# Kernel tuning notes

Measured on AMD Instinct MI355X. Metric: run time of the kernel, lower is better.

Reference implementation:

```python
import jax, jax.numpy as jnp
import numpy as np

LN_EPS = 1e-5


def setup_inputs() -> dict:
    key = jax.random.key(0)
    ks = jax.random.split(key, 4)
    B, S, H, R = 8, 4096, 1024, 64
    hidden_states = jax.random.normal(ks[0], (B, S, H), dtype=jnp.float32)
    w_down = jax.random.normal(ks[1], (H, R), dtype=jnp.float32) * (1.0 / np.sqrt(H))
    b_down = jnp.zeros((R,), dtype=jnp.float32)
    w_up = jax.random.normal(ks[2], (R, H), dtype=jnp.float32) * (1.0 / np.sqrt(R))
    b_up = jnp.zeros((H,), dtype=jnp.float32)
    ln_gamma = jnp.ones((H,), dtype=jnp.float32)
    ln_beta = jnp.zeros((H,), dtype=jnp.float32)
    return {
        "hidden_states": hidden_states,
        "ln_gamma": ln_gamma,
        "ln_beta": ln_beta,
        "w_down": w_down,
        "b_down": b_down,
        "w_up": w_up,
        "b_up": b_up,
    }


def _layernorm(x, gamma, beta):
    mu = jnp.mean(x, axis=-1, keepdims=True)
    var = jnp.mean(jnp.square(x - mu), axis=-1, keepdims=True)
    return (x - mu) * jax.lax.rsqrt(var + LN_EPS) * gamma + beta


def reference(hidden_states, ln_gamma, ln_beta, w_down, b_down, w_up, b_up):
    # pre-norm adapter: LN -> down-proj -> gelu -> up-proj -> +residual
    res = hidden_states
    h = _layernorm(hidden_states, ln_gamma, ln_beta)
    h = jnp.einsum("bsh,hr->bsr", h, w_down) + b_down
    h = jax.nn.gelu(h, approximate=False)  # torch GELU (exact erf form)
    h = jnp.einsum("bsr,rh->bsh", h, w_up) + b_up
    return h + res
```

## Files before the change

### kernel.cpp

```cpp
#include <hip/hip_runtime.h>
#include <hip/hip_bf16.h>
#include <math.h>

#define H 1024
#define R 64
#define NTHREADS 256
#define TSTRIDE 72

typedef __attribute__((ext_vector_type(8))) short short8;
typedef __attribute__((ext_vector_type(4))) float floatx4;

__device__ __forceinline__ unsigned short f2bf(float f) {
    unsigned int u = __builtin_bit_cast(unsigned int, f);
    u += 0x7fffu + ((u >> 16) & 1u);
    return (unsigned short)(u >> 16);
}

__global__ void prep(const float* __restrict__ w_down,
                     const float* __restrict__ w_up,
                     const float* __restrict__ gamma,
                     const float* __restrict__ beta,
                     const float* __restrict__ b_down,
                     unsigned short* __restrict__ wsd,
                     unsigned short* __restrict__ wsu,
                     float* __restrict__ w1, float* __restrict__ c0) {
    __shared__ float red[8];
    int bid = blockIdx.x;
    if (bid < 256) {
        int tid = bid * NTHREADS + threadIdx.x;
        int j    = tid & 7;
        int lane = (tid >> 3) & 63;
        int f    = tid >> 9;
        int b = lane >> 4, p = lane & 15;
        {
            int kk = f >> 2, n = f & 3;
            int row = kk * 32 + b * 8 + j;
            int col = n * 16 + p;
            wsd[tid] = f2bf(gamma[row] * w_down[row * R + col]);
        }
        {
            int ks = f >> 6, n = f & 63;
            int row = ks * 32 + b * 8 + j;
            int col = n * 16 + p;
            wsu[tid] = f2bf(w_up[row * H + col]);
        }
    } else {
        int r = bid - 256;
        int t = threadIdx.x;
        float a = 0.f, c = 0.f;
        for (int h = t; h < H; h += NTHREADS) {
            float wd = w_down[h * R + r];
            a += gamma[h] * wd;
            c += beta[h] * wd;
        }
        #pragma unroll
        for (int off = 32; off >= 1; off >>= 1) {
            a += __shfl_xor(a, off);
            c += __shfl_xor(c, off);
        }
        int wv = t >> 6;
        if ((t & 63) == 0) { red[wv] = a; red[4 + wv] = c; }
        __syncthreads();
        if (t == 0) {
            w1[r] = red[0] + red[1] + red[2] + red[3];
            c0[r] = red[4] + red[5] + red[6] + red[7] + b_down[r];
        }
    }
}

__global__ __launch_bounds__(NTHREADS, 2)
void adapter_kernel(const float* __restrict__ x,
                    const float* __restrict__ b_up,
                    const unsigned short* __restrict__ wsd,
                    const unsigned short* __restrict__ wsu,
                    const float* __restrict__ w1v,
                    const float* __restrict__ c0v,
                    float* __restrict__ out) {
    __shared__ __align__(16) unsigned short t_lds[4][16 * TSTRIDE];

    const int tid  = threadIdx.x;
    const int lane = tid & 63;
    const int w    = tid >> 6;
    const int p    = lane & 15;
    const int b    = lane >> 4;
    const long row0 = (long)blockIdx.x * 64 + w * 16;

    float s1 = 0.f, s2 = 0.f;
    floatx4 acc[4];
    #pragma unroll
    for (int nt = 0; nt < 4; ++nt) acc[nt] = floatx4{0.f, 0.f, 0.f, 0.f};

    const float* xw = x + (row0 + p) * H + b * 8;
    const short8* wsd8 = (const short8*)wsd;

    floatx4 bx0[8], bx1[8];
    short8 wd[2][4];
    #pragma unroll
    for (int i = 0; i < 8; ++i) {
        bx0[i] = *(const floatx4*)(xw + i * 32);
        bx1[i] = *(const floatx4*)(xw + i * 32 + 4);
    }
    #pragma unroll
    for (int nt = 0; nt < 4; ++nt) {
        wd[0][nt] = wsd8[(size_t)nt * 64 + lane];
        wd[1][nt] = wsd8[(size_t)(4 + nt) * 64 + lane];
    }

    for (int ko = 0; ko < 3; ++ko) {
        #pragma unroll
        for (int ki = 0; ki < 8; ++ki) {
            const int kt = ko * 8 + ki;
            floatx4 v0 = bx0[ki], v1 = bx1[ki];
            bx0[ki] = *(const floatx4*)(xw + (kt + 8) * 32);
            bx1[ki] = *(const floatx4*)(xw + (kt + 8) * 32 + 4);
            short8 wl[4];
            #pragma unroll
            for (int nt = 0; nt < 4; ++nt) {
                wl[nt] = wd[ki & 1][nt];
                wd[ki & 1][nt] = wsd8[(size_t)((kt + 2) * 4 + nt) * 64 + lane];
            }
            short8 a;
            #pragma unroll
            for (int e = 0; e < 4; ++e) {
                s1 += v0[e] + v1[e];
                s2 += v0[e] * v0[e] + v1[e] * v1[e];
                a[e]     = (short)f2bf(v0[e]);
                a[4 + e] = (short)f2bf(v1[e]);
            }
            #pragma unroll
            for (int nt = 0; nt < 4; ++nt)
                acc[nt] = __builtin_amdgcn_mfma_f32_16x16x32_bf16(a, wl[nt], acc[nt], 0, 0, 0);
        }
    }
    #pragma unroll
    for (int ki = 0; ki < 8; ++ki) {
        const int kt = 24 + ki;
        floatx4 v0 = bx0[ki], v1 = bx1[ki];
        short8 wl[4];
        #pragma unroll
        for (int nt = 0; nt < 4; ++nt) {
            wl[nt] = wd[ki & 1][nt];
            if (ki < 6)
                wd[ki & 1][nt] = wsd8[(size_t)((kt + 2) * 4 + nt) * 64 + lane];
        }
        short8 a;
        #pragma unroll
        for (int e = 0; e < 4; ++e) {
            s1 += v0[e] + v1[e];
            s2 += v0[e] * v0[e] + v1[e] * v1[e];
            a[e]     = (short)f2bf(v0[e]);
            a[4 + e] = (short)f2bf(v1[e]);
        }
        #pragma unroll
        for (int nt = 0; nt < 4; ++nt)
            acc[nt] = __builtin_amdgcn_mfma_f32_16x16x32_bf16(a, wl[nt], acc[nt], 0, 0, 0);
    }

    s1 += __shfl_xor(s1, 16); s1 += __shfl_xor(s1, 32);
    s2 += __shfl_xor(s2, 16); s2 += __shfl_xor(s2, 32);
    float mu = s1 * (1.0f / (float)H);
    float var = s2 * (1.0f / (float)H) - mu * mu;
    float rs = rsqrtf(var + 1e-5f);

    #pragma unroll
    for (int reg = 0; reg < 4; ++reg) {
        float mur = __shfl(mu, b * 4 + reg);
        float rsr = __shfl(rs, b * 4 + reg);
        #pragma unroll
        for (int nt = 0; nt < 4; ++nt) {
            int col = nt * 16 + p;
            float u = rsr * (acc[nt][reg] - mur * w1v[col]) + c0v[col];
            u = 0.5f * u * (1.0f + erff(u * 0.70710678f));
            t_lds[w][(b * 4 + reg) * TSTRIDE + col] = f2bf(u);
        }
    }

    const short8* wsu8 = (const short8*)wsu;
    const long rbase = row0 + b * 4;
    short8 wq0[8], wq1[8];
    float bb[8], rx0[8], rx1[8], rx2[8], rx3[8];
    #pragma unroll
    for (int i = 0; i < 8; ++i) {
        wq0[i] = wsu8[(size_t)i * 64 + lane];
        wq1[i] = wsu8[(size_t)(64 + i) * 64 + lane];
        int col = i * 16 + p;
        bb[i]  = b_up[col];
        rx0[i] = x[(rbase + 0) * H + col];
        rx1[i] = x[(rbase + 1) * H + col];
        rx2[i] = x[(rbase + 2) * H + col];
        rx3[i] = x[(rbase + 3) * H + col];
    }
    __syncthreads();
    short8 a0 = *(const short8*)&t_lds[w][p * TSTRIDE + b * 8];
    short8 a1 = *(const short8*)&t_lds[w][p * TSTRIDE + 32 + b * 8];

    for (int no = 0; no < 7; ++no) {
        #pragma unroll
        for (int ni = 0; ni < 8; ++ni) {
            const int n = no * 8 + ni;
            short8 bu0 = wq0[ni], bu1 = wq1[ni];
            float bup = bb[ni];
            float r0 = rx0[ni], r1 = rx1[ni], r2 = rx2[ni], r3 = rx3[ni];
            const int nc = n + 8;
            const int colc = nc * 16 + p;
            wq0[ni] = wsu8[(size_t)nc * 64 + lane];
            wq1[ni] = wsu8[(size_t)(64 + nc) * 64 + lane];
            bb[ni]  = b_up[colc];
            rx0[ni] = x[(rbase + 0) * H + colc];
            rx1[ni] = x[(rbase + 1) * H + colc];
            rx2[ni] = x[(rbase + 2) * H + colc];
            rx3[ni] = x[(rbase + 3) * H + colc];
            floatx4 av = {0.f, 0.f, 0.f, 0.f};
            av = __builtin_amdgcn_mfma_f32_16x16x32_bf16(a0, bu0, av, 0, 0, 0);
            av = __builtin_amdgcn_mfma_f32_16x16x32_bf16(a1, bu1, av, 0, 0, 0);
            const int col = n * 16 + p;
            out[(rbase + 0) * H + col] = av[0] + bup + r0;
            out[(rbase + 1) * H + col] = av[1] + bup + r1;
            out[(rbase + 2) * H + col] = av[2] + bup + r2;
            out[(rbase + 3) * H + col] = av[3] + bup + r3;
        }
    }
    #pragma unroll
    for (int ni = 0; ni < 8; ++ni) {
        const int n = 56 + ni;
        short8 bu0 = wq0[ni], bu1 = wq1[ni];
        floatx4 av = {0.f, 0.f, 0.f, 0.f};
        av = __builtin_amdgcn_mfma_f32_16x16x32_bf16(a0, bu0, av, 0, 0, 0);
        av = __builtin_amdgcn_mfma_f32_16x16x32_bf16(a1, bu1, av, 0, 0, 0);
        const int col = n * 16 + p;
        out[(rbase + 0) * H + col] = av[0] + bb[ni] + rx0[ni];
        out[(rbase + 1) * H + col] = av[1] + bb[ni] + rx1[ni];
        out[(rbase + 2) * H + col] = av[2] + bb[ni] + rx2[ni];
        out[(rbase + 3) * H + col] = av[3] + bb[ni] + rx3[ni];
    }
}

extern "C" void kernel_launch(void* const* d_in, const int* in_sizes, int n_in,
                              void* d_out, int out_size, void* d_ws, size_t ws_size,
                              hipStream_t stream) {
    const float* x      = (const float*)d_in[0];
    const float* gamma  = (const float*)d_in[1];
    const float* beta   = (const float*)d_in[2];
    const float* w_down = (const float*)d_in[3];
    const float* b_down = (const float*)d_in[4];
    const float* w_up   = (const float*)d_in[5];
    const float* b_up   = (const float*)d_in[6];
    float* out = (float*)d_out;

    unsigned short* wsd = (unsigned short*)d_ws;
    unsigned short* wsu = wsd + 65536;
    float* w1 = (float*)(wsu + 65536);
    float* c0 = w1 + 64;

    int M = in_sizes[0] / H;
    prep<<<320, NTHREADS, 0, stream>>>(w_down, w_up, gamma, beta, b_down,
                                       wsd, wsu, w1, c0);
    adapter_kernel<<<M / 64, NTHREADS, 0, stream>>>(x, b_up, wsd, wsu, w1, c0, out);
}
```

Before: 278.2 us.

## Stage adapter weights through double-buffered LDS via global_load_lds

Down- and up-projection weight fragments are now loaded cooperatively into double-buffered LDS with the direct global-to-LDS load builtin. Each wave previously fetched every weight fragment itself into registers. This cuts redundant global/L2 weight traffic across the four waves and frees registers that held prefetched weights. In exchange it adds a __syncthreads per chunk, uses 32KB more LDS (which may lower occupancy), and shortens the x prefetch depth in the down-projection loop.

```diff
diff --git a/kernel.cpp b/kernel.cpp
--- a/kernel.cpp
+++ b/kernel.cpp
@@ -9,6 +9,10 @@
 
 typedef __attribute__((ext_vector_type(8))) short short8;
 typedef __attribute__((ext_vector_type(4))) float floatx4;
+
+#define GLD_LDS(gp, lp) \
+    __builtin_amdgcn_global_load_lds((const __attribute__((address_space(1))) void*)(gp), \
+                                     (__attribute__((address_space(3))) void*)(lp), 16, 0, 0)
 
 __device__ __forceinline__ unsigned short f2bf(float f) {
     unsigned int u = __builtin_bit_cast(unsigned int, f);
@@ -76,6 +80,7 @@
                     const float* __restrict__ w1v,
                     const float* __restrict__ c0v,
                     float* __restrict__ out) {
+    __shared__ __align__(16) unsigned short wbuf[2][8192];
     __shared__ __align__(16) unsigned short t_lds[4][16 * TSTRIDE];
 
     const int tid  = threadIdx.x;
@@ -84,76 +89,62 @@
     const int p    = lane & 15;
     const int b    = lane >> 4;
     const long row0 = (long)blockIdx.x * 64 + w * 16;
+    const float* xw = x + (row0 + p) * H + b * 8;
 
     float s1 = 0.f, s2 = 0.f;
     floatx4 acc[4];
     #pragma unroll
     for (int nt = 0; nt < 4; ++nt) acc[nt] = floatx4{0.f, 0.f, 0.f, 0.f};
 
-    const float* xw = x + (row0 + p) * H + b * 8;
-    const short8* wsd8 = (const short8*)wsd;
-
-    floatx4 bx0[8], bx1[8];
-    short8 wd[2][4];
-    #pragma unroll
-    for (int i = 0; i < 8; ++i) {
-        bx0[i] = *(const floatx4*)(xw + i * 32);
-        bx1[i] = *(const floatx4*)(xw + i * 32 + 4);
-    }
-    #pragma unroll
-    for (int nt = 0; nt < 4; ++nt) {
-        wd[0][nt] = wsd8[(size_t)nt * 64 + lane];
-        wd[1][nt] = wsd8[(size_t)(4 + nt) * 64 + lane];
-    }
-
-    for (int ko = 0; ko < 3; ++ko) {
-        #pragma unroll
-        for (int ki = 0; ki < 8; ++ki) {
-            const int kt = ko * 8 + ki;
-            floatx4 v0 = bx0[ki], v1 = bx1[ki];
-            bx0[ki] = *(const floatx4*)(xw + (kt + 8) * 32);
-            bx1[ki] = *(const floatx4*)(xw + (kt + 8) * 32 + 4);
-            short8 wl[4];
-            #pragma unroll
-            for (int nt = 0; nt < 4; ++nt) {
-                wl[nt] = wd[ki & 1][nt];
-                wd[ki & 1][nt] = wsd8[(size_t)((kt + 2) * 4 + nt) * 64 + lane];
-            }
+    auto stage_d = [&](int c, int buf) {
+        #pragma unroll
+        for (int i = 0; i < 4; ++i) {
+            int fl = w * 4 + i;
+            GLD_LDS(wsd + ((size_t)(c * 16 + fl) * 64 + lane) * 8,
+                    &wbuf[buf][fl * 512]);
+        }
+    };
+    auto loadx = [&](int c, floatx4* v0, floatx4* v1) {
+        #pragma unroll
+        for (int i = 0; i < 4; ++i) {
+            v0[i] = *(const floatx4*)(xw + (c * 4 + i) * 32);
+            v1[i] = *(const floatx4*)(xw + (c * 4 + i) * 32 + 4);
+        }
+    };
+    auto compute_d = [&](const floatx4* v0, const floatx4* v1,
+                         const unsigned short* wb) {
+        #pragma unroll
+        for (int i = 0; i < 4; ++i) {
             short8 a;
             #pragma unroll
             for (int e = 0; e < 4; ++e) {
-                s1 += v0[e] + v1[e];
-                s2 += v0[e] * v0[e] + v1[e] * v1[e];
-                a[e]     = (short)f2bf(v0[e]);
-                a[4 + e] = (short)f2bf(v1[e]);
+                float f0 = v0[i][e], f1 = v1[i][e];
+                s1 += f0 + f1;
+                s2 += f0 * f0 + f1 * f1;
+                a[e]     = (short)f2bf(f0);
+                a[4 + e] = (short)f2bf(f1);
             }
             #pragma unroll
             for (int nt = 0; nt < 4; ++nt)
-                acc[nt] = __builtin_amdgcn_mfma_f32_16x16x32_bf16(a, wl[nt], acc[nt], 0, 0, 0);
-        }
-    }
-    #pragma unroll
-    for (int ki = 0; ki < 8; ++ki) {
-        const int kt = 24 + ki;
-        floatx4 v0 = bx0[ki], v1 = bx1[ki];
-        short8 wl[4];
-        #pragma unroll
-        for (int nt = 0; nt < 4; ++nt) {
-            wl[nt] = wd[ki & 1][nt];
-            if (ki < 6)
-                wd[ki & 1][nt] = wsd8[(size_t)((kt + 2) * 4 + nt) * 64 + lane];
-        }
-        short8 a;
-        #pragma unroll
-        for (int e = 0; e < 4; ++e) {
-            s1 += v0[e] + v1[e];
-            s2 += v0[e] * v0[e] + v1[e] * v1[e];
-            a[e]     = (short)f2bf(v0[e]);
-            a[4 + e] = (short)f2bf(v1[e]);
-        }
-        #pragma unroll
-        for (int nt = 0; nt < 4; ++nt)
-            acc[nt] = __builtin_amdgcn_mfma_f32_16x16x32_bf16(a, wl[nt], acc[nt], 0, 0, 0);
+                acc[nt] = __builtin_amdgcn_mfma_f32_16x16x32_bf16(
+                    a, *(const short8*)&wb[(i * 4 + nt) * 512 + lane * 8],
+                    acc[nt], 0, 0, 0);
+        }
+    };
+
+    floatx4 xA0[4], xA1[4], xB0[4], xB1[4];
+    stage_d(0, 0);
+    loadx(0, xA0, xA1);
+    __syncthreads();
+    #pragma unroll
+    for (int c = 0; c < 8; ++c) {
+        if (c + 1 < 8) {
+            if (((c + 1) & 1) == 1) { stage_d(c + 1, 1); loadx(c + 1, xB0, xB1); }
+            else                    { stage_d(c + 1, 0); loadx(c + 1, xA0, xA1); }
+        }
+        if ((c & 1) == 0) compute_d(xA0, xA1, wbuf[0]);
+        else              compute_d(xB0, xB1, wbuf[1]);
+        __syncthreads();
     }
 
     s1 += __shfl_xor(s1, 16); s1 += __shfl_xor(s1, 32);
@@ -175,14 +166,22 @@
         }
     }
 
-    const short8* wsu8 = (const short8*)wsu;
     const long rbase = row0 + b * 4;
-    short8 wq0[8], wq1[8];
-    float bb[8], rx0[8], rx1[8], rx2[8], rx3[8];
+    auto stage_u = [&](int c, int buf) {
+        #pragma unroll
+        for (int i = 0; i < 2; ++i) {
+            int nl = w * 2 + i;
+            GLD_LDS(wsu + ((size_t)(c * 8 + nl) * 64 + lane) * 8,
+                    &wbuf[buf][nl * 512]);
+            GLD_LDS(wsu + ((size_t)(64 + c * 8 + nl) * 64 + lane) * 8,
+                    &wbuf[buf][4096 + nl * 512]);
+        }
+    };
+
+    stage_u(0, 0);
+    float rx0[8], rx1[8], rx2[8], rx3[8], bb[8];
     #pragma unroll
     for (int i = 0; i < 8; ++i) {
-        wq0[i] = wsu8[(size_t)i * 64 + lane];
-        wq1[i] = wsu8[(size_t)(64 + i) * 64 + lane];
         int col = i * 16 + p;
         bb[i]  = b_up[col];
         rx0[i] = x[(rbase + 0) * H + col];
@@ -194,44 +193,38 @@
     short8 a0 = *(const short8*)&t_lds[w][p * TSTRIDE + b * 8];
     short8 a1 = *(const short8*)&t_lds[w][p * TSTRIDE + 32 + b * 8];
 
-    for (int no = 0; no < 7; ++no) {
+    auto up_chunk = [&](int c, const unsigned short* wb) {
         #pragma unroll
         for (int ni = 0; ni < 8; ++ni) {
-            const int n = no * 8 + ni;
-            short8 bu0 = wq0[ni], bu1 = wq1[ni];
-            float bup = bb[ni];
-            float r0 = rx0[ni], r1 = rx1[ni], r2 = rx2[ni], r3 = rx3[ni];
-            const int nc = n + 8;
-            const int colc = nc * 16 + p;
-            wq0[ni] = wsu8[(size_t)nc * 64 + lane];
-            wq1[ni] = wsu8[(size_t)(64 + nc) * 64 + lane];
-            bb[ni]  = b_up[colc];
-            rx0[ni] = x[(rbase + 0) * H + colc];
-            rx1[ni] = x[(rbase + 1) * H + colc];
-            rx2[ni] = x[(rbase + 2) * H + colc];
-            rx3[ni] = x[(rbase + 3) * H + colc];
+            const int n = c * 8 + ni;
+            short8 bu0 = *(const short8*)&wb[ni * 512 + lane * 8];
+            short8 bu1 = *(const short8*)&wb[4096 + ni * 512 + lane * 8];
             floatx4 av = {0.f, 0.f, 0.f, 0.f};
             av = __builtin_amdgcn_mfma_f32_16x16x32_bf16(a0, bu0, av, 0, 0, 0);
             av = __builtin_amdgcn_mfma_f32_16x16x32_bf16(a1, bu1, av, 0, 0, 0);
             const int col = n * 16 + p;
+            float bup = bb[ni], r0 = rx0[ni], r1 = rx1[ni], r2 = rx2[ni], r3 = rx3[ni];
+            if (n + 8 < 64) {
+                const int colc = (n + 8) * 16 + p;
+                bb[ni]  = b_up[colc];
+                rx0[ni] = x[(rbase + 0) * H + colc];
+                rx1[ni] = x[(rbase + 1) * H + colc];
+                rx2[ni] = x[(rbase + 2) * H + colc];
+                rx3[ni] = x[(rbase + 3) * H + colc];
+            }
             out[(rbase + 0) * H + col] = av[0] + bup + r0;
             out[(rbase + 1) * H + col] = av[1] + bup + r1;
             out[(rbase + 2) * H + col] = av[2] + bup + r2;
             out[(rbase + 3) * H + col] = av[3] + bup + r3;
         }
-    }
-    #pragma unroll
-    for (int ni = 0; ni < 8; ++ni) {
-        const int n = 56 + ni;
-        short8 bu0 = wq0[ni], bu1 = wq1[ni];
-        floatx4 av = {0.f, 0.f, 0.f, 0.f};
-        av = __builtin_amdgcn_mfma_f32_16x16x32_bf16(a0, bu0, av, 0, 0, 0);
-        av = __builtin_amdgcn_mfma_f32_16x16x32_bf16(a1, bu1, av, 0, 0, 0);
-        const int col = n * 16 + p;
-        out[(rbase + 0) * H + col] = av[0] + bb[ni] + rx0[ni];
-        out[(rbase + 1) * H + col] = av[1] + bb[ni] + rx1[ni];
-        out[(rbase + 2) * H + col] = av[2] + bb[ni] + rx2[ni];
-        out[(rbase + 3) * H + col] = av[3] + bb[ni] + rx3[ni];
+    };
+
+    #pragma unroll
+    for (int c = 0; c < 8; ++c) {
+        if (c + 1 < 8) stage_u(c + 1, (c + 1) & 1);
+        if ((c & 1) == 0) up_chunk(c, wbuf[0]);
+        else              up_chunk(c, wbuf[1]);
+        if (c + 1 < 8) __syncthreads();
     }
 }
 
```

Result: no change. 280.3 us (+0.8%).
